# Kernel optimization log

Measured on AMD Instinct MI355X. Metric: run time of the kernel, lower is better.

Reference implementation:

```python
import jax, jax.numpy as jnp
import numpy as np

N = 8192
IN_F = 256
OUT_F = 128
ALPHA = 0.2
NEG = -9000000000000000.0

def setup_inputs() -> dict:
    key = jax.random.key(0)
    k1, k2, k3, k4 = jax.random.split(key, 4)
    h = jax.random.normal(k1, (N, IN_F), dtype=jnp.float32)
    adj = jax.random.randint(k2, (N, N), 0, 2, dtype=jnp.int32)
    # xavier-uniform-like params
    limW = float(np.sqrt(6.0 / (IN_F + OUT_F)))
    W = jax.random.uniform(k3, (IN_F, OUT_F), minval=-limW, maxval=limW, dtype=jnp.float32)
    lima = float(np.sqrt(6.0 / (2 * OUT_F + 1)))
    a = jax.random.uniform(k4, (2 * OUT_F, 1), minval=-lima, maxval=lima, dtype=jnp.float32)
    return {"h": h, "adj": adj, "W": W, "a": a}

def reference(h, adj, W, a):
    Wh = h @ W  # [N, F]
    # e_ij = LeakyReLU(a1.Wh_i + a2.Wh_j) -- avoids [N,N,2F] intermediate
    a1 = a[:OUT_F, 0]  # [F]
    a2 = a[OUT_F:, 0]  # [F]
    f1 = Wh @ a1  # [N]
    f2 = Wh @ a2  # [N]
    e = jax.nn.leaky_relu(f1[:, None] + f2[None, :], negative_slope=ALPHA)  # [N,N]
    att = jnp.where(adj > 0, e, jnp.float32(NEG))
    att = jax.nn.softmax(att, axis=1)
    h_prime = att @ Wh  # [N, F]
    return h_prime
```

## Files before the change

### kernel.cpp

```cpp
#include <hip/hip_runtime.h>
#include <hip/hip_bf16.h>

#define N    8192
#define INF  256
#define OUTF 128
#define ALPHA 0.2f
#define JS   8
#define NTS  (N / JS / 32)

typedef __attribute__((ext_vector_type(8))) short bf16x8;
typedef __attribute__((ext_vector_type(4))) float f32x4;

__device__ __forceinline__ unsigned short f2bf(float x) {
    union { float f; unsigned u; } v; v.f = x;
    unsigned r = v.u + 0x7fff + ((v.u >> 16) & 1);
    return (unsigned short)(r >> 16);
}

__device__ __forceinline__ void gll16(const void* g, void* l) {
    __builtin_amdgcn_global_load_lds(
        (const __attribute__((address_space(1))) unsigned*)g,
        (__attribute__((address_space(3))) unsigned*)l, 16, 0, 0);
}

__device__ __forceinline__ unsigned pack8(int4 a, int4 b) {
    return (a.x > 0 ?   1u : 0u) | (a.y > 0 ?   2u : 0u)
         | (a.z > 0 ?   4u : 0u) | (a.w > 0 ?   8u : 0u)
         | (b.x > 0 ?  16u : 0u) | (b.y > 0 ?  32u : 0u)
         | (b.z > 0 ?  64u : 0u) | (b.w > 0 ? 128u : 0u);
}

__global__ __launch_bounds__(256) void k1_prep(
        const float* __restrict__ h, const float* __restrict__ W,
        const float* __restrict__ a,
        unsigned short* __restrict__ WhTb, float* __restrict__ f1, float* __restrict__ f2) {
    __shared__ float hs[8][INF];
    const int t = threadIdx.x;

    const int i0 = blockIdx.x * 8;
    #pragma unroll
    for (int u = 0; u < 2; ++u) {
        int idx = u * 256 + t;
        int r   = idx >> 6;
        int kq  = idx & 63;
        *(float4*)&hs[r][kq * 4] = *(const float4*)(h + (size_t)(i0 + r) * INF + kq * 4);
    }
    __syncthreads();

    const int rg = t >> 5;
    const int ct = t & 31;
    float acc[4] = {0.f, 0.f, 0.f, 0.f};

    #pragma unroll 8
    for (int k = 0; k < INF; ++k) {
        float4 wv = *(const float4*)(W + (size_t)k * OUTF + ct * 4);
        float  hx = hs[rg][k];
        acc[0] += hx * wv.x; acc[1] += hx * wv.y;
        acc[2] += hx * wv.z; acc[3] += hx * wv.w;
    }

    const int r0 = i0 + rg;
    const int jb = r0 >> 5;
    const int jo = r0 & 31;
    #pragma unroll
    for (int cc = 0; cc < 4; ++cc)
        WhTb[(size_t)jb * 4096 + (ct * 4 + cc) * 32 + jo] = f2bf(acc[cc]);

    const float4 a1v = *(const float4*)(a + ct * 4);
    const float4 a2v = *(const float4*)(a + OUTF + ct * 4);
    float p1 = acc[0]*a1v.x + acc[1]*a1v.y + acc[2]*a1v.z + acc[3]*a1v.w;
    float p2 = acc[0]*a2v.x + acc[1]*a2v.y + acc[2]*a2v.z + acc[3]*a2v.w;
    #pragma unroll
    for (int off = 16; off > 0; off >>= 1) {
        p1 += __shfl_down(p1, off, 32);
        p2 += __shfl_down(p2, off, 32);
    }
    if (ct == 0) { f1[r0] = p1; f2[r0] = p2; }
}

__device__ __forceinline__ float pbit(float f1r, float fv, unsigned byte_,
                                      int u, float& dsum) {
    float s = f1r + fv;
    float e = fmaxf(s, ALPHA * s);
    float p = (byte_ & (1u << u)) ? __expf(e) : 0.f;
    dsum += p;
    return p;
}

#define VMB6 "s_waitcnt vmcnt(6)\n\ts_barrier"
#define VMB2 "s_waitcnt vmcnt(2)\n\ts_barrier"

#define K2STEP(O, JT, VMB, ISSG, ISSA)                                       \
    {                                                                        \
        int4 na_ = {}, nb_ = {};                                             \
        if (ISSA) { na_ = arow[((JT) + 1) * 8]; nb_ = arow[((JT) + 1) * 8 + 1]; } \
        if (ISSG) {                                                          \
            const char* ws_ = (const char*)WhTb + (size_t)(tile0 + (JT) + 2) * 8192; \
            char* bd_ = (char*)&bsm[((O) + 2) & 3][0];                       \
            gll16(ws_ + tsw,        bd_ + wv * 1024);                        \
            gll16(ws_ + 4096 + tsw, bd_ + 4096 + wv * 1024);                 \
        }                                                                    \
        float4 F0_ = *(const float4*)&f2s[(JT) * 32 + quad * 8];             \
        float4 F1_ = *(const float4*)&f2s[(JT) * 32 + quad * 8 + 4];         \
        unsigned byte_ = byteC;                                              \
        float p0_ = pbit(f1r, F0_.x, byte_, 0, dsum);                        \
        float p1_ = pbit(f1r, F0_.y, byte_, 1, dsum);                        \
        float p2_ = pbit(f1r, F0_.z, byte_, 2, dsum);                        \
        float p3_ = pbit(f1r, F0_.w, byte_, 3, dsum);                        \
        float p4_ = pbit(f1r, F1_.x, byte_, 4, dsum);                        \
        float p5_ = pbit(f1r, F1_.y, byte_, 5, dsum);                        \
        float p6_ = pbit(f1r, F1_.z, byte_, 6, dsum);                        \
        float p7_ = pbit(f1r, F1_.w, byte_, 7, dsum);                        \
        union { __hip_bfloat162 hh[4]; bf16x8 v; } pk_;                      \
        pk_.hh[0] = __float22bfloat162_rn(make_float2(p0_, p1_));            \
        pk_.hh[1] = __float22bfloat162_rn(make_float2(p2_, p3_));            \
        pk_.hh[2] = __float22bfloat162_rn(make_float2(p4_, p5_));            \
        pk_.hh[3] = __float22bfloat162_rn(make_float2(p6_, p7_));            \
        bf16x8 afrag = pk_.v;                                                \
        asm volatile(VMB ::: "memory");                                      \
        const char* bb_ = (const char*)&bsm[(O)][0] + laneb2;                \
        bf16x8 b0_ = *(const bf16x8*)(bb_);                                  \
        bf16x8 b1_ = *(const bf16x8*)(bb_ + 1024);                           \
        bf16x8 b2_ = *(const bf16x8*)(bb_ + 2048);                           \
        bf16x8 b3_ = *(const bf16x8*)(bb_ + 3072);                           \
        bf16x8 b4_ = *(const bf16x8*)(bb_ + 4096);                           \
        bf16x8 b5_ = *(const bf16x8*)(bb_ + 5120);                           \
        bf16x8 b6_ = *(const bf16x8*)(bb_ + 6144);                           \
        bf16x8 b7_ = *(const bf16x8*)(bb_ + 7168);                           \
        acc0 = __builtin_amdgcn_mfma_f32_16x16x32_bf16(afrag, b0_, acc0, 0, 0, 0); \
        acc1 = __builtin_amdgcn_mfma_f32_16x16x32_bf16(afrag, b1_, acc1, 0, 0, 0); \
        acc2 = __builtin_amdgcn_mfma_f32_16x16x32_bf16(afrag, b2_, acc2, 0, 0, 0); \
        acc3 = __builtin_amdgcn_mfma_f32_16x16x32_bf16(afrag, b3_, acc3, 0, 0, 0); \
        acc4 = __builtin_amdgcn_mfma_f32_16x16x32_bf16(afrag, b4_, acc4, 0, 0, 0); \
        acc5 = __builtin_amdgcn_mfma_f32_16x16x32_bf16(afrag, b5_, acc5, 0, 0, 0); \
        acc6 = __builtin_amdgcn_mfma_f32_16x16x32_bf16(afrag, b6_, acc6, 0, 0, 0); \
        acc7 = __builtin_amdgcn_mfma_f32_16x16x32_bf16(afrag, b7_, acc7, 0, 0, 0); \
        if (ISSA) byteC = pack8(na_, nb_);                                   \
    }

__global__ __launch_bounds__(256, 4) void k2_attn(
        const int* __restrict__ adj, const unsigned short* __restrict__ WhTb,
        const float* __restrict__ f1, const float* __restrict__ f2,
        float* __restrict__ num, float* __restrict__ den) {
    __shared__ unsigned short bsm[4][4096];
    __shared__ float f2s[1024];

    const int t    = threadIdx.x;
    const int wv   = t >> 6;
    const int ln   = t & 63;
    const int m16  = ln & 15;
    const int quad = ln >> 4;
    const int i0   = blockIdx.x * 64;
    const int s    = blockIdx.y;
    const int row  = i0 + wv * 16 + m16;
    const int tile0 = s * NTS;
    const int j0    = s * (N / JS);
    const int laneb2 = m16 * 64 + ((quad ^ ((m16 >> 1) & 3)) << 4);
    const int tsw = (t * 16) ^ (((t >> 3) & 3) << 4);

    const int4* arow = (const int4*)(adj + (size_t)row * N + j0 + quad * 8);

    int4 na0 = arow[0], nb0 = arow[1];
    *(float4*)&f2s[t * 4] = *(const float4*)(f2 + j0 + t * 4);
    {
        const char* ws0 = (const char*)WhTb + (size_t)tile0 * 8192;
        char* bd0 = (char*)&bsm[0][0];
        gll16(ws0 + tsw,        bd0 + wv * 1024);
        gll16(ws0 + 4096 + tsw, bd0 + 4096 + wv * 1024);
        const char* ws1 = ws0 + 8192;
        char* bd1 = (char*)&bsm[1][0];
        gll16(ws1 + tsw,        bd1 + wv * 1024);
        gll16(ws1 + 4096 + tsw, bd1 + 4096 + wv * 1024);
    }

    const float f1r = f1[row];

    f32x4 acc0 = {0.f,0.f,0.f,0.f}, acc1 = {0.f,0.f,0.f,0.f};
    f32x4 acc2 = {0.f,0.f,0.f,0.f}, acc3 = {0.f,0.f,0.f,0.f};
    f32x4 acc4 = {0.f,0.f,0.f,0.f}, acc5 = {0.f,0.f,0.f,0.f};
    f32x4 acc6 = {0.f,0.f,0.f,0.f}, acc7 = {0.f,0.f,0.f,0.f};
    float dsum = 0.f;

    unsigned byteC = pack8(na0, nb0);
    asm volatile("s_waitcnt lgkmcnt(0)\n\ts_barrier" ::: "memory");

    for (int g = 0; g < 7; ++g) {
        const int jtb = g * 4;
        K2STEP(0, jtb + 0, VMB6, 1, 1)
        K2STEP(1, jtb + 1, VMB6, 1, 1)
        K2STEP(2, jtb + 2, VMB6, 1, 1)
        K2STEP(3, jtb + 3, VMB6, 1, 1)
    }
    K2STEP(0, 28, VMB6, 1, 1)
    K2STEP(1, 29, VMB6, 1, 1)
    K2STEP(2, 30, VMB6, 0, 1)
    K2STEP(3, 31, VMB2, 0, 0)

    dsum += __shfl_xor(dsum, 16);
    dsum += __shfl_xor(dsum, 32);
    if (quad == 0) den[(size_t)s * N + row] = dsum;

    float* np = num + (size_t)s * N * OUTF;
    #pragma unroll
    for (int r = 0; r < 4; ++r) {
        const size_t orow = (size_t)(i0 + wv * 16 + quad * 4 + r) * OUTF;
        np[orow + 0 * 16 + m16] = acc0[r];
        np[orow + 1 * 16 + m16] = acc1[r];
        np[orow + 2 * 16 + m16] = acc2[r];
        np[orow + 3 * 16 + m16] = acc3[r];
        np[orow + 4 * 16 + m16] = acc4[r];
        np[orow + 5 * 16 + m16] = acc5[r];
        np[orow + 6 * 16 + m16] = acc6[r];
        np[orow + 7 * 16 + m16] = acc7[r];
    }
}

__global__ __launch_bounds__(256) void k3_combine(
        const float* __restrict__ num, const float* __restrict__ den,
        float* __restrict__ out) {
    const int idx = blockIdx.x * 256 + threadIdx.x;
    const int row = idx >> 5;
    const int c4  = (idx & 31) * 4;
    float4 ns = {0.f,0.f,0.f,0.f};
    float  ds = 0.f;
    #pragma unroll
    for (int s = 0; s < JS; ++s) {
        float4 nv = *(const float4*)(num + ((size_t)s * N + row) * OUTF + c4);
        ns.x += nv.x; ns.y += nv.y; ns.z += nv.z; ns.w += nv.w;
        ds += den[(size_t)s * N + row];
    }
    const float inv = 1.0f / ds;
    float4 o = {ns.x * inv, ns.y * inv, ns.z * inv, ns.w * inv};
    *(float4*)(out + (size_t)row * OUTF + c4) = o;
}

extern "C" void kernel_launch(void* const* d_in, const int* in_sizes, int n_in,
                              void* d_out, int out_size, void* d_ws, size_t ws_size,
                              hipStream_t stream) {
    const float* h   = (const float*)d_in[0];
    const int*   adj = (const int*)  d_in[1];
    const float* W   = (const float*)d_in[2];
    const float* a   = (const float*)d_in[3];
    float* out = (float*)d_out;

    unsigned short* WhTb = (unsigned short*)d_ws;
    float*    f1   = (float*)(WhTb + (size_t)N * OUTF);
    float*    f2   = f1 + N;
    float*    den  = f2 + N;
    float*    num  = den + (size_t)JS * N;

    k1_prep   <<<N / 8, 256, 0, stream>>>(h, W, a, WhTb, f1, f2);
    k2_attn   <<<dim3(N / 64, JS), 256, 0, stream>>>(adj, WhTb, f1, f2, num, den);
    k3_combine<<<(N * OUTF / 4) / 256, 256, 0, stream>>>(num, den, out);
}
```

Baseline: 453.3 us.

## Split key range across waves in-block and fuse combine into attention kernel

Each block now handles 32 rows, with each of its four waves covering a quarter of the key columns for two 16-row tiles. Per-wave WhT tiles are double-buffered in private LDS regions, so no block barriers are needed in the main loop. The partial numerators and denominators are reduced in shared memory at the end and the normalized output is written directly. This removes the separate combine kernel and the global num/den round trip. In exchange the kernel uses 96KB of LDS at occupancy 1, giving 256 blocks, and each wave holds more accumulator registers.

```diff
diff --git a/kernel.cpp b/kernel.cpp
--- a/kernel.cpp
+++ b/kernel.cpp
@@ -5,8 +5,6 @@
 #define INF  256
 #define OUTF 128
 #define ALPHA 0.2f
-#define JS   8
-#define NTS  (N / JS / 32)
 
 typedef __attribute__((ext_vector_type(8))) short bf16x8;
 typedef __attribute__((ext_vector_type(4))) float f32x4;
@@ -87,38 +85,57 @@
     return p;
 }
 
-#define VMB6 "s_waitcnt vmcnt(6)\n\ts_barrier"
-#define VMB2 "s_waitcnt vmcnt(2)\n\ts_barrier"
-
-#define K2STEP(O, JT, VMB, ISSG, ISSA)                                       \
+#define STAGE8(SRC, DST)                                                     \
+    gll16((SRC),        (DST));        gll16((SRC) + 1024, (DST) + 1024);    \
+    gll16((SRC) + 2048, (DST) + 2048); gll16((SRC) + 3072, (DST) + 3072);    \
+    gll16((SRC) + 4096, (DST) + 4096); gll16((SRC) + 5120, (DST) + 5120);    \
+    gll16((SRC) + 6144, (DST) + 6144); gll16((SRC) + 7168, (DST) + 7168);
+
+#define STEP(O, JT, VMN, ISSG, ISSA, PACK)                                   \
     {                                                                        \
-        int4 na_ = {}, nb_ = {};                                             \
-        if (ISSA) { na_ = arow[((JT) + 1) * 8]; nb_ = arow[((JT) + 1) * 8 + 1]; } \
+        asm volatile("s_waitcnt lgkmcnt(0)" ::: "memory");                   \
+        if (ISSA) {                                                          \
+            const int ai_ = ((JT) + 2) * 8 + quad * 2;                       \
+            if ((O) == 0) { eA0 = adjA[ai_]; eA1 = adjA[ai_ + 1];            \
+                            eB0 = adjB[ai_]; eB1 = adjB[ai_ + 1]; }          \
+            else          { oA0 = adjA[ai_]; oA1 = adjA[ai_ + 1];            \
+                            oB0 = adjB[ai_]; oB1 = adjB[ai_ + 1]; }          \
+        }                                                                    \
         if (ISSG) {                                                          \
-            const char* ws_ = (const char*)WhTb + (size_t)(tile0 + (JT) + 2) * 8192; \
-            char* bd_ = (char*)&bsm[((O) + 2) & 3][0];                       \
-            gll16(ws_ + tsw,        bd_ + wv * 1024);                        \
-            gll16(ws_ + 4096 + tsw, bd_ + 4096 + wv * 1024);                 \
+            const char* ws_ = (const char*)WhTb + (size_t)(tbase + (JT) + 1) * 8192 + lsw; \
+            char* bd_ = rbase + (((O) ^ 1) ? 8192 : 0);                      \
+            STAGE8(ws_, bd_)                                                 \
         }                                                                    \
-        float4 F0_ = *(const float4*)&f2s[(JT) * 32 + quad * 8];             \
-        float4 F1_ = *(const float4*)&f2s[(JT) * 32 + quad * 8 + 4];         \
-        unsigned byte_ = byteC;                                              \
-        float p0_ = pbit(f1r, F0_.x, byte_, 0, dsum);                        \
-        float p1_ = pbit(f1r, F0_.y, byte_, 1, dsum);                        \
-        float p2_ = pbit(f1r, F0_.z, byte_, 2, dsum);                        \
-        float p3_ = pbit(f1r, F0_.w, byte_, 3, dsum);                        \
-        float p4_ = pbit(f1r, F1_.x, byte_, 4, dsum);                        \
-        float p5_ = pbit(f1r, F1_.y, byte_, 5, dsum);                        \
-        float p6_ = pbit(f1r, F1_.z, byte_, 6, dsum);                        \
-        float p7_ = pbit(f1r, F1_.w, byte_, 7, dsum);                        \
-        union { __hip_bfloat162 hh[4]; bf16x8 v; } pk_;                      \
-        pk_.hh[0] = __float22bfloat162_rn(make_float2(p0_, p1_));            \
-        pk_.hh[1] = __float22bfloat162_rn(make_float2(p2_, p3_));            \
-        pk_.hh[2] = __float22bfloat162_rn(make_float2(p4_, p5_));            \
-        pk_.hh[3] = __float22bfloat162_rn(make_float2(p6_, p7_));            \
-        bf16x8 afrag = pk_.v;                                                \
-        asm volatile(VMB ::: "memory");                                      \
-        const char* bb_ = (const char*)&bsm[(O)][0] + laneb2;                \
+        float4 F0_ = *(const float4*)&f2s[jw + (JT) * 32 + quad * 8];        \
+        float4 F1_ = *(const float4*)&f2s[jw + (JT) * 32 + quad * 8 + 4];    \
+        float a0_ = pbit(f1A, F0_.x, byteCA, 0, dsA);                        \
+        float a1_ = pbit(f1A, F0_.y, byteCA, 1, dsA);                        \
+        float a2_ = pbit(f1A, F0_.z, byteCA, 2, dsA);                        \
+        float a3_ = pbit(f1A, F0_.w, byteCA, 3, dsA);                        \
+        float a4_ = pbit(f1A, F1_.x, byteCA, 4, dsA);                        \
+        float a5_ = pbit(f1A, F1_.y, byteCA, 5, dsA);                        \
+        float a6_ = pbit(f1A, F1_.z, byteCA, 6, dsA);                        \
+        float a7_ = pbit(f1A, F1_.w, byteCA, 7, dsA);                        \
+        float c0_ = pbit(f1B, F0_.x, byteCB, 0, dsB);                        \
+        float c1_ = pbit(f1B, F0_.y, byteCB, 1, dsB);                        \
+        float c2_ = pbit(f1B, F0_.z, byteCB, 2, dsB);                        \
+        float c3_ = pbit(f1B, F0_.w, byteCB, 3, dsB);                        \
+        float c4_ = pbit(f1B, F1_.x, byteCB, 4, dsB);                        \
+        float c5_ = pbit(f1B, F1_.y, byteCB, 5, dsB);                        \
+        float c6_ = pbit(f1B, F1_.z, byteCB, 6, dsB);                        \
+        float c7_ = pbit(f1B, F1_.w, byteCB, 7, dsB);                        \
+        union { __hip_bfloat162 hh[4]; bf16x8 v; } pkA_, pkB_;               \
+        pkA_.hh[0] = __float22bfloat162_rn(make_float2(a0_, a1_));           \
+        pkA_.hh[1] = __float22bfloat162_rn(make_float2(a2_, a3_));           \
+        pkA_.hh[2] = __float22bfloat162_rn(make_float2(a4_, a5_));           \
+        pkA_.hh[3] = __float22bfloat162_rn(make_float2(a6_, a7_));           \
+        pkB_.hh[0] = __float22bfloat162_rn(make_float2(c0_, c1_));           \
+        pkB_.hh[1] = __float22bfloat162_rn(make_float2(c2_, c3_));           \
+        pkB_.hh[2] = __float22bfloat162_rn(make_float2(c4_, c5_));           \
+        pkB_.hh[3] = __float22bfloat162_rn(make_float2(c6_, c7_));           \
+        bf16x8 afA = pkA_.v, afB = pkB_.v;                                   \
+        asm volatile("s_waitcnt vmcnt(" #VMN ")" ::: "memory");              \
+        const char* bb_ = rbase + ((O) ? 8192 : 0) + laneb2;                 \
         bf16x8 b0_ = *(const bf16x8*)(bb_);                                  \
         bf16x8 b1_ = *(const bf16x8*)(bb_ + 1024);                           \
         bf16x8 b2_ = *(const bf16x8*)(bb_ + 2048);                           \
@@ -127,111 +144,138 @@
         bf16x8 b5_ = *(const bf16x8*)(bb_ + 5120);                           \
         bf16x8 b6_ = *(const bf16x8*)(bb_ + 6144);                           \
         bf16x8 b7_ = *(const bf16x8*)(bb_ + 7168);                           \
-        acc0 = __builtin_amdgcn_mfma_f32_16x16x32_bf16(afrag, b0_, acc0, 0, 0, 0); \
-        acc1 = __builtin_amdgcn_mfma_f32_16x16x32_bf16(afrag, b1_, acc1, 0, 0, 0); \
-        acc2 = __builtin_amdgcn_mfma_f32_16x16x32_bf16(afrag, b2_, acc2, 0, 0, 0); \
-        acc3 = __builtin_amdgcn_mfma_f32_16x16x32_bf16(afrag, b3_, acc3, 0, 0, 0); \
-        acc4 = __builtin_amdgcn_mfma_f32_16x16x32_bf16(afrag, b4_, acc4, 0, 0, 0); \
-        acc5 = __builtin_amdgcn_mfma_f32_16x16x32_bf16(afrag, b5_, acc5, 0, 0, 0); \
-        acc6 = __builtin_amdgcn_mfma_f32_16x16x32_bf16(afrag, b6_, acc6, 0, 0, 0); \
-        acc7 = __builtin_amdgcn_mfma_f32_16x16x32_bf16(afrag, b7_, acc7, 0, 0, 0); \
-        if (ISSA) byteC = pack8(na_, nb_);                                   \
-    }
-
-__global__ __launch_bounds__(256, 4) void k2_attn(
+        acA0 = __builtin_amdgcn_mfma_f32_16x16x32_bf16(afA, b0_, acA0, 0, 0, 0); \
+        acB0 = __builtin_amdgcn_mfma_f32_16x16x32_bf16(afB, b0_, acB0, 0, 0, 0); \
+        acA1 = __builtin_amdgcn_mfma_f32_16x16x32_bf16(afA, b1_, acA1, 0, 0, 0); \
+        acB1 = __builtin_amdgcn_mfma_f32_16x16x32_bf16(afB, b1_, acB1, 0, 0, 0); \
+        acA2 = __builtin_amdgcn_mfma_f32_16x16x32_bf16(afA, b2_, acA2, 0, 0, 0); \
+        acB2 = __builtin_amdgcn_mfma_f32_16x16x32_bf16(afB, b2_, acB2, 0, 0, 0); \
+        acA3 = __builtin_amdgcn_mfma_f32_16x16x32_bf16(afA, b3_, acA3, 0, 0, 0); \
+        acB3 = __builtin_amdgcn_mfma_f32_16x16x32_bf16(afB, b3_, acB3, 0, 0, 0); \
+        acA4 = __builtin_amdgcn_mfma_f32_16x16x32_bf16(afA, b4_, acA4, 0, 0, 0); \
+        acB4 = __builtin_amdgcn_mfma_f32_16x16x32_bf16(afB, b4_, acB4, 0, 0, 0); \
+        acA5 = __builtin_amdgcn_mfma_f32_16x16x32_bf16(afA, b5_, acA5, 0, 0, 0); \
+        acB5 = __builtin_amdgcn_mfma_f32_16x16x32_bf16(afB, b5_, acB5, 0, 0, 0); \
+        acA6 = __builtin_amdgcn_mfma_f32_16x16x32_bf16(afA, b6_, acA6, 0, 0, 0); \
+        acB6 = __builtin_amdgcn_mfma_f32_16x16x32_bf16(afB, b6_, acB6, 0, 0, 0); \
+        acA7 = __builtin_amdgcn_mfma_f32_16x16x32_bf16(afA, b7_, acA7, 0, 0, 0); \
+        acB7 = __builtin_amdgcn_mfma_f32_16x16x32_bf16(afB, b7_, acB7, 0, 0, 0); \
+        if (PACK) {                                                          \
+            if ((O) == 0) { byteCA = pack8(oA0, oA1); byteCB = pack8(oB0, oB1); } \
+            else          { byteCA = pack8(eA0, eA1); byteCB = pack8(eB0, eB1); } \
+        }                                                                    \
+    }
+
+__global__ __launch_bounds__(256, 1) void k2_attn(
         const int* __restrict__ adj, const unsigned short* __restrict__ WhTb,
         const float* __restrict__ f1, const float* __restrict__ f2,
-        float* __restrict__ num, float* __restrict__ den) {
-    __shared__ unsigned short bsm[4][4096];
-    __shared__ float f2s[1024];
+        float* __restrict__ out) {
+    __shared__ __align__(16) char smem[98304];
+    float* f2s = (float*)(smem + 65536);
 
     const int t    = threadIdx.x;
     const int wv   = t >> 6;
     const int ln   = t & 63;
     const int m16  = ln & 15;
     const int quad = ln >> 4;
-    const int i0   = blockIdx.x * 64;
-    const int s    = blockIdx.y;
-    const int row  = i0 + wv * 16 + m16;
-    const int tile0 = s * NTS;
-    const int j0    = s * (N / JS);
+    const int i0   = blockIdx.x * 32;
+    const int rowA = i0 + m16;
+    const int rowB = i0 + 16 + m16;
+    const int jw   = wv * 2048;
+    const int tbase = wv * 64;
+    char* rbase = smem + wv * 16384;
     const int laneb2 = m16 * 64 + ((quad ^ ((m16 >> 1) & 3)) << 4);
-    const int tsw = (t * 16) ^ (((t >> 3) & 3) << 4);
-
-    const int4* arow = (const int4*)(adj + (size_t)row * N + j0 + quad * 8);
-
-    int4 na0 = arow[0], nb0 = arow[1];
-    *(float4*)&f2s[t * 4] = *(const float4*)(f2 + j0 + t * 4);
+    const int lsw = (ln * 16) ^ (((ln >> 3) & 3) << 4);
+
     {
-        const char* ws0 = (const char*)WhTb + (size_t)tile0 * 8192;
-        char* bd0 = (char*)&bsm[0][0];
-        gll16(ws0 + tsw,        bd0 + wv * 1024);
-        gll16(ws0 + 4096 + tsw, bd0 + 4096 + wv * 1024);
-        const char* ws1 = ws0 + 8192;
-        char* bd1 = (char*)&bsm[1][0];
-        gll16(ws1 + tsw,        bd1 + wv * 1024);
-        gll16(ws1 + 4096 + tsw, bd1 + 4096 + wv * 1024);
-    }
-
-    const float f1r = f1[row];
-
-    f32x4 acc0 = {0.f,0.f,0.f,0.f}, acc1 = {0.f,0.f,0.f,0.f};
-    f32x4 acc2 = {0.f,0.f,0.f,0.f}, acc3 = {0.f,0.f,0.f,0.f};
-    f32x4 acc4 = {0.f,0.f,0.f,0.f}, acc5 = {0.f,0.f,0.f,0.f};
-    f32x4 acc6 = {0.f,0.f,0.f,0.f}, acc7 = {0.f,0.f,0.f,0.f};
-    float dsum = 0.f;
-
-    unsigned byteC = pack8(na0, nb0);
-    asm volatile("s_waitcnt lgkmcnt(0)\n\ts_barrier" ::: "memory");
-
-    for (int g = 0; g < 7; ++g) {
-        const int jtb = g * 4;
-        K2STEP(0, jtb + 0, VMB6, 1, 1)
-        K2STEP(1, jtb + 1, VMB6, 1, 1)
-        K2STEP(2, jtb + 2, VMB6, 1, 1)
-        K2STEP(3, jtb + 3, VMB6, 1, 1)
-    }
-    K2STEP(0, 28, VMB6, 1, 1)
-    K2STEP(1, 29, VMB6, 1, 1)
-    K2STEP(2, 30, VMB6, 0, 1)
-    K2STEP(3, 31, VMB2, 0, 0)
-
-    dsum += __shfl_xor(dsum, 16);
-    dsum += __shfl_xor(dsum, 32);
-    if (quad == 0) den[(size_t)s * N + row] = dsum;
-
-    float* np = num + (size_t)s * N * OUTF;
+        const float4* f2g4 = (const float4*)f2;
+        float4* f2s4 = (float4*)f2s;
+        #pragma unroll
+        for (int u = 0; u < 8; ++u) f2s4[u * 256 + t] = f2g4[u * 256 + t];
+    }
+    const float f1A = f1[rowA];
+    const float f1B = f1[rowB];
+    __syncthreads();
+
+    const int4* adjA = (const int4*)(adj + (size_t)rowA * N + jw);
+    const int4* adjB = (const int4*)(adj + (size_t)rowB * N + jw);
+    int4 eA0 = {}, eA1 = {}, eB0 = {}, eB1 = {};
+    int4 pA0 = adjA[quad * 2], pA1 = adjA[quad * 2 + 1];
+    int4 pB0 = adjB[quad * 2], pB1 = adjB[quad * 2 + 1];
+    int4 oA0 = adjA[8 + quad * 2], oA1 = adjA[8 + quad * 2 + 1];
+    int4 oB0 = adjB[8 + quad * 2], oB1 = adjB[8 + quad * 2 + 1];
+    {
+        const char* ws0 = (const char*)WhTb + (size_t)tbase * 8192 + lsw;
+        STAGE8(ws0, rbase)
+    }
+    unsigned byteCA = pack8(pA0, pA1);
+    unsigned byteCB = pack8(pB0, pB1);
+
+    f32x4 acA0 = {0.f,0.f,0.f,0.f}, acA1 = {0.f,0.f,0.f,0.f};
+    f32x4 acA2 = {0.f,0.f,0.f,0.f}, acA3 = {0.f,0.f,0.f,0.f};
+    f32x4 acA4 = {0.f,0.f,0.f,0.f}, acA5 = {0.f,0.f,0.f,0.f};
+    f32x4 acA6 = {0.f,0.f,0.f,0.f}, acA7 = {0.f,0.f,0.f,0.f};
+    f32x4 acB0 = {0.f,0.f,0.f,0.f}, acB1 = {0.f,0.f,0.f,0.f};
+    f32x4 acB2 = {0.f,0.f,0.f,0.f}, acB3 = {0.f,0.f,0.f,0.f};
+    f32x4 acB4 = {0.f,0.f,0.f,0.f}, acB5 = {0.f,0.f,0.f,0.f};
+    f32x4 acB6 = {0.f,0.f,0.f,0.f}, acB7 = {0.f,0.f,0.f,0.f};
+    float dsA = 0.f, dsB = 0.f;
+
+    for (int g = 0; g < 31; ++g) {
+        const int jt = g * 2;
+        STEP(0, jt,     12, 1, 1, 1)
+        STEP(1, jt + 1, 12, 1, 1, 1)
+    }
+    STEP(0, 62, 8, 1, 0, 1)
+    STEP(1, 63, 0, 0, 0, 0)
+
+    float* nl = (float*)rbase;
     #pragma unroll
     for (int r = 0; r < 4; ++r) {
-        const size_t orow = (size_t)(i0 + wv * 16 + quad * 4 + r) * OUTF;
-        np[orow + 0 * 16 + m16] = acc0[r];
-        np[orow + 1 * 16 + m16] = acc1[r];
-        np[orow + 2 * 16 + m16] = acc2[r];
-        np[orow + 3 * 16 + m16] = acc3[r];
-        np[orow + 4 * 16 + m16] = acc4[r];
-        np[orow + 5 * 16 + m16] = acc5[r];
-        np[orow + 6 * 16 + m16] = acc6[r];
-        np[orow + 7 * 16 + m16] = acc7[r];
-    }
-}
-
-__global__ __launch_bounds__(256) void k3_combine(
-        const float* __restrict__ num, const float* __restrict__ den,
-        float* __restrict__ out) {
-    const int idx = blockIdx.x * 256 + threadIdx.x;
-    const int row = idx >> 5;
-    const int c4  = (idx & 31) * 4;
-    float4 ns = {0.f,0.f,0.f,0.f};
-    float  ds = 0.f;
-    #pragma unroll
-    for (int s = 0; s < JS; ++s) {
-        float4 nv = *(const float4*)(num + ((size_t)s * N + row) * OUTF + c4);
-        ns.x += nv.x; ns.y += nv.y; ns.z += nv.z; ns.w += nv.w;
-        ds += den[(size_t)s * N + row];
-    }
-    const float inv = 1.0f / ds;
-    float4 o = {ns.x * inv, ns.y * inv, ns.z * inv, ns.w * inv};
-    *(float4*)(out + (size_t)row * OUTF + c4) = o;
+        const int ra = quad * 4 + r;
+        nl[ra * 128 + 0 * 16 + m16] = acA0[r];
+        nl[ra * 128 + 1 * 16 + m16] = acA1[r];
+        nl[ra * 128 + 2 * 16 + m16] = acA2[r];
+        nl[ra * 128 + 3 * 16 + m16] = acA3[r];
+        nl[ra * 128 + 4 * 16 + m16] = acA4[r];
+        nl[ra * 128 + 5 * 16 + m16] = acA5[r];
+        nl[ra * 128 + 6 * 16 + m16] = acA6[r];
+        nl[ra * 128 + 7 * 16 + m16] = acA7[r];
+        nl[(16 + ra) * 128 + 0 * 16 + m16] = acB0[r];
+        nl[(16 + ra) * 128 + 1 * 16 + m16] = acB1[r];
+        nl[(16 + ra) * 128 + 2 * 16 + m16] = acB2[r];
+        nl[(16 + ra) * 128 + 3 * 16 + m16] = acB3[r];
+        nl[(16 + ra) * 128 + 4 * 16 + m16] = acB4[r];
+        nl[(16 + ra) * 128 + 5 * 16 + m16] = acB5[r];
+        nl[(16 + ra) * 128 + 6 * 16 + m16] = acB6[r];
+        nl[(16 + ra) * 128 + 7 * 16 + m16] = acB7[r];
+    }
+    dsA += __shfl_xor(dsA, 16); dsA += __shfl_xor(dsA, 32);
+    dsB += __shfl_xor(dsB, 16); dsB += __shfl_xor(dsB, 32);
+    __syncthreads();
+    float* denl = f2s;
+    if (quad == 0) {
+        denl[wv * 32 + m16]      = dsA;
+        denl[wv * 32 + 16 + m16] = dsB;
+    }
+    __syncthreads();
+
+    const int row = t >> 3;
+    const int c0  = (t & 7) * 16;
+    const float den = denl[row] + denl[32 + row] + denl[64 + row] + denl[96 + row];
+    const float inv = 1.0f / den;
+    float* op = out + (size_t)(i0 + row) * OUTF + c0;
+    #pragma unroll
+    for (int k = 0; k < 4; ++k) {
+        float4 sv = {0.f, 0.f, 0.f, 0.f};
+        #pragma unroll
+        for (int w = 0; w < 4; ++w) {
+            const float4 v = *(const float4*)((const float*)(smem + w * 16384) + row * 128 + c0 + k * 4);
+            sv.x += v.x; sv.y += v.y; sv.z += v.z; sv.w += v.w;
+        }
+        float4 o = {sv.x * inv, sv.y * inv, sv.z * inv, sv.w * inv};
+        *(float4*)(op + k * 4) = o;
+    }
 }
 
 extern "C" void kernel_launch(void* const* d_in, const int* in_sizes, int n_in,
@@ -244,12 +288,9 @@
     float* out = (float*)d_out;
 
     unsigned short* WhTb = (unsigned short*)d_ws;
-    float*    f1   = (float*)(WhTb + (size_t)N * OUTF);
-    float*    f2   = f1 + N;
-    float*    den  = f2 + N;
-    float*    num  = den + (size_t)JS * N;
-
-    k1_prep   <<<N / 8, 256, 0, stream>>>(h, W, a, WhTb, f1, f2);
-    k2_attn   <<<dim3(N / 64, JS), 256, 0, stream>>>(adj, WhTb, f1, f2, num, den);
-    k3_combine<<<(N * OUTF / 4) / 256, 256, 0, stream>>>(num, den, out);
-}
+    float* f1 = (float*)(WhTb + (size_t)N * OUTF);
+    float* f2 = f1 + N;
+
+    k1_prep <<<N / 8, 256, 0, stream>>>(h, W, a, WhTb, f1, f2);
+    k2_attn <<<N / 32, 256, 0, stream>>>(adj, WhTb, f1, f2, out);
+}
```

Result: faster. 443.9 us (-2.1%).
